# Optimization experiments

Measured on AMD Instinct MI355X. Metric: run time of the kernel, lower is better.

## Reference

```python
import jax, jax.numpy as jnp
from jax import lax
import numpy as np

ALPHA = 100.0  # NetVLAD beta

def _avg_pool2(x):
    # AvgPool2d(2, stride=2) on NCHW
    s = lax.reduce_window(x, 0.0, lax.add, (1, 1, 2, 2), (1, 1, 2, 2), 'VALID')
    return s * 0.25

def _conv3x3(x, w, b):
    y = lax.conv_general_dilated(x, w, (1, 1), 'SAME',
                                 dimension_numbers=('NCHW', 'OIHW', 'NCHW'))
    return y + b[None, :, None, None]

def _l2norm(v, axis):
    return v / jnp.maximum(jnp.linalg.norm(v, axis=axis, keepdims=True), 1e-12)


def setup_inputs() -> dict:
    key = jax.random.key(0)
    ks = jax.random.split(key, 10)
    N, H, W = 16, 512, 512
    K, D = 64, 16          # clusters, NetVLAD feature dim (conv2 out channels)
    T, E, Hd = 64, 300, 512  # caption len, emb dim (rnn_inp=rnn_out), rnn_hid
    img = jax.random.normal(ks[0], (N, 3, H, W), jnp.float32)
    cap = jax.random.normal(ks[1], (N, T, E), jnp.float32)
    conv1_w = jax.random.normal(ks[2], (4, 3, 3, 3), jnp.float32) * 0.1
    conv1_b = jnp.zeros((4,), jnp.float32)
    conv2_w = jax.random.normal(ks[3], (16, 4, 3, 3), jnp.float32) * 0.1
    conv2_b = jnp.zeros((16,), jnp.float32)
    centroids = jax.random.uniform(ks[4], (K, D), jnp.float32)  # torch.rand init
    nv_w = 2.0 * ALPHA * centroids                     # 1x1 conv weight, squeezed [K,D]
    nv_b = -ALPHA * jnp.linalg.norm(centroids, axis=1)  # [K]
    fc_w = jax.random.normal(ks[5], (Hd, K * D), jnp.float32) * 0.02
    fc_b = jnp.zeros((Hd,), jnp.float32)
    hid_w = jax.random.normal(ks[6], (Hd, E + Hd), jnp.float32) * 0.02
    hid_b = jnp.zeros((Hd,), jnp.float32)
    out_w = jax.random.normal(ks[7], (E, Hd), jnp.float32) * 0.02
    out_b = jnp.zeros((E,), jnp.float32)
    return dict(img=img, cap=cap, conv1_w=conv1_w, conv1_b=conv1_b,
                conv2_w=conv2_w, conv2_b=conv2_b, centroids=centroids,
                nv_w=nv_w, nv_b=nv_b, fc_w=fc_w, fc_b=fc_b,
                hid_w=hid_w, hid_b=hid_b, out_w=out_w, out_b=out_b)


def reference(img, cap, conv1_w, conv1_b, conv2_w, conv2_b, centroids,
              nv_w, nv_b, fc_w, fc_b, hid_w, hid_b, out_w, out_b):
    # CNN encoder
    x = jax.nn.relu(_conv3x3(img, conv1_w, conv1_b))
    x = _avg_pool2(x)
    x = jax.nn.relu(_conv3x3(x, conv2_w, conv2_b))
    x = _avg_pool2(x)                      # [N, 16, 128, 128]
    N, C = x.shape[0], x.shape[1]
    xf = x.reshape(N, C, -1)               # [N, C, HW]
    # NetVLAD: 1x1 conv -> softmax over clusters
    soft_assign = jnp.einsum('kc,nch->nkh', nv_w, xf) + nv_b[None, :, None]
    soft_assign = jax.nn.softmax(soft_assign, axis=1)  # [N, K, HW]
    # algebraic two-matmul form of sum_hw a[n,k,hw]*(x[n,c,hw]-centroids[k,c])
    a_sum = soft_assign.sum(axis=-1)                      # [N, K]
    vlad = jnp.einsum('nkh,nch->nkc', soft_assign, xf)    # [N, K, C]
    vlad = vlad - a_sum[:, :, None] * centroids[None]     # [N, K, C]
    vlad = _l2norm(vlad, axis=2)
    vlad = vlad.reshape(N, -1)
    vlad = _l2norm(vlad, axis=1)
    features = vlad @ fc_w.T + fc_b                        # [N, rnn_hid]
    # RNN decoder on sample 0
    feat0 = features[0]
    cap0 = cap[0]                                          # [T, E]

    def step(carry, x_t):
        h, x_in = carry
        comb = jnp.concatenate([x_in, h])
        h_new = jax.nn.sigmoid(hid_w @ comb + hid_b)
        y = jax.nn.sigmoid(out_w @ h_new + out_b)
        return (h_new, x_t), y

    (_, ys) = lax.scan(step, (feat0, cap0[0]), cap0[1:])
    output = jnp.concatenate([cap0[:1], ys], axis=0)       # [T, E]
    loss = jnp.mean((output - cap0) ** 2)
    return loss
```

## Files before the change

kernel.cpp:

```cpp
#include <hip/hip_runtime.h>
#include <math.h>


#define POISON 0xAAAAAAAAu
#define MAGIC  0x13579BDFu

__device__ __forceinline__ float sigmoidf_(float x) {
  return 1.0f / (1.0f + __expf(-x));
}
__device__ __forceinline__ unsigned uld(const unsigned* p) {
  return __hip_atomic_load(p, __ATOMIC_RELAXED, __HIP_MEMORY_SCOPE_AGENT);
}
__device__ __forceinline__ float fld(const float* p) {
  return __hip_atomic_load(p, __ATOMIC_RELAXED, __HIP_MEMORY_SCOPE_AGENT);
}
__device__ __forceinline__ void fst(float* p, float v) {
  __hip_atomic_store(p, v, __ATOMIC_RELAXED, __HIP_MEMORY_SCOPE_AGENT);
}
__device__ __forceinline__ void ust(unsigned* p, unsigned v) {
  __hip_atomic_store(p, v, __ATOMIC_RELAXED, __HIP_MEMORY_SCOPE_AGENT);
}

__global__ __launch_bounds__(256, 1)
void k_front(const float* __restrict__ img,  const float* __restrict__ cap,
             const float* __restrict__ c1w,  const float* __restrict__ c1b,
             const float* __restrict__ c2w,  const float* __restrict__ c2b,
             const float* __restrict__ cent, const float* __restrict__ nvw,
             const float* __restrict__ nvb,  const float* __restrict__ fcw,
             const float* __restrict__ fcb,  const float* __restrict__ hidw,
             const float* __restrict__ hidb,
             float* __restrict__ p1,   float* __restrict__ vacc,
             float* __restrict__ asum, float* __restrict__ feat,
             float* __restrict__ U,    float* __restrict__ H,
             unsigned* __restrict__ flags, float* __restrict__ loss) {
  __shared__ __align__(16) float smem[12832];
  const int bx  = blockIdx.x;
  const int tid = threadIdx.x;
  unsigned* flag_magic = flags + 0;
  unsigned* conv_done  = flags + 1;
  unsigned* vlad_done  = flags + 2;

  if (bx < 63) {
    const int t = bx;
    float* csh = smem;
    if (tid < 256) csh[tid] = cap[t * 300 + tid];
    if (tid < 44) csh[256 + tid] = cap[t * 300 + 256 + tid];
    __syncthreads();
    #pragma unroll
    for (int rr = 0; rr < 2; ++rr) {
      int row = tid + rr * 256;
      float acc = hidb[row];
      const float4* w4 = (const float4*)(hidw + row * 812);
      const float4* c4 = (const float4*)csh;
      #pragma unroll 5
      for (int i = 0; i < 75; ++i) {
        float4 aa = w4[i]; float4 xx = c4[i];
        acc = fmaf(aa.x, xx.x, acc); acc = fmaf(aa.y, xx.y, acc);
        acc = fmaf(aa.z, xx.z, acc); acc = fmaf(aa.w, xx.w, acc);
      }
      U[t * 512 + row] = acc;
    }
    return;
  }

  if (bx < 71) {
    const int q = bx - 63;
    if (tid == 0) {
      while (uld(vlad_done) != 64u) __builtin_amdgcn_s_sleep(8);
    }
    __syncthreads();
    float* v  = smem;
    float* rn = smem + 1024;
    float* fr = smem + 1088;
    for (int i = tid; i < 1024; i += 256)
      v[i] = fld(vacc + i) - fld(asum + (i >> 4)) * cent[i];
    __syncthreads();
    if (tid < 64) {
      float ss = 0.f;
      #pragma unroll
      for (int c = 0; c < 16; ++c) { float xx = v[tid * 16 + c]; ss = fmaf(xx, xx, ss); }
      rn[tid] = fmaxf(sqrtf(ss), 1e-12f);
    }
    __syncthreads();
    float gs = 0.f;
    for (int i = tid; i < 1024; i += 256) {
      float nv = v[i] / rn[i >> 4];
      v[i] = nv;
      gs = fmaf(nv, nv, gs);
    }
    #pragma unroll
    for (int o = 32; o > 0; o >>= 1) gs += __shfl_down(gs, o);
    if ((tid & 63) == 0) fr[tid >> 6] = gs;
    __syncthreads();
    if (tid == 0) {
      float tot = fr[0] + fr[1] + fr[2] + fr[3];
      fr[8] = 1.0f / fmaxf(sqrtf(tot), 1e-12f);
    }
    __syncthreads();
    float invg = fr[8];
    int row = q * 64 + (tid >> 2);
    int cg = tid & 3;
    float acc = 0.f;
    const float4* fw4 = (const float4*)(fcw + row * 1024 + cg * 256);
    const float4* v4  = (const float4*)(v + cg * 256);
    #pragma unroll 4
    for (int i = 0; i < 64; ++i) {
      float4 aa = fw4[i]; float4 xx = v4[i];
      acc = fmaf(aa.x, xx.x, acc); acc = fmaf(aa.y, xx.y, acc);
      acc = fmaf(aa.z, xx.z, acc); acc = fmaf(aa.w, xx.w, acc);
    }
    acc += __shfl_xor(acc, 1);
    acc += __shfl_xor(acc, 2);
    if (cg == 0) feat[row] = fmaf(invg, acc, fcb[row]);
    return;
  }

  if (bx < 135) {
    const int vb = bx - 71;
    float* ps  = smem;
    float* xs  = smem + 8320;
    float* wsh = smem + 10880;
    float* bsh = smem + 11904;
    float* aS  = smem + 11968;
    float* cw  = smem + 12224;
    float* cb  = smem + 12800;
    for (int i = tid; i < 1024; i += 256) wsh[i] = nvw[i];
    if (tid < 64) bsh[tid] = nvb[tid];
    for (int i = tid; i < 576; i += 256) cw[i] = c2w[i];
    if (tid < 16) cb[tid] = c2b[tid];
    if (tid == 0) {
      while (uld(conv_done) != 121u) __builtin_amdgcn_s_sleep(4);
    }
    __syncthreads();
    int ox = tid & 127;
    int oy = vb * 2 + (tid >> 7);
    int y0 = oy * 2 - 1, x0 = ox * 2 - 1;
    float a[16][4];
    #pragma unroll
    for (int oc = 0; oc < 16; ++oc) {
      float bb = cb[oc];
      a[oc][0] = bb; a[oc][1] = bb; a[oc][2] = bb; a[oc][3] = bb;
    }
    #pragma unroll
    for (int ci = 0; ci < 4; ++ci) {
      float P[4][4];
      #pragma unroll
      for (int j = 0; j < 4; ++j) {
        int y = y0 + j;
        #pragma unroll
        for (int i = 0; i < 4; ++i) {
          int x = x0 + i;
          bool ok = ((unsigned)y < 256u) && ((unsigned)x < 256u);
          P[j][i] = ok ? fld(p1 + ci * 65536 + y * 256 + x) : 0.0f;
        }
      }
      #pragma unroll
      for (int oc = 0; oc < 16; ++oc) {
        #pragma unroll
        for (int ky = 0; ky < 3; ++ky) {
          #pragma unroll
          for (int kx = 0; kx < 3; ++kx) {
            float wv = cw[oc * 36 + ci * 9 + ky * 3 + kx];
            a[oc][0] = fmaf(wv, P[ky][kx],         a[oc][0]);
            a[oc][1] = fmaf(wv, P[ky][kx + 1],     a[oc][1]);
            a[oc][2] = fmaf(wv, P[ky + 1][kx],     a[oc][2]);
            a[oc][3] = fmaf(wv, P[ky + 1][kx + 1], a[oc][3]);
          }
        }
      }
    }
    float x[16];
    #pragma unroll
    for (int oc = 0; oc < 16; ++oc)
      x[oc] = 0.25f * (fmaxf(a[oc][0], 0.f) + fmaxf(a[oc][1], 0.f) +
                       fmaxf(a[oc][2], 0.f) + fmaxf(a[oc][3], 0.f));
    float p[64];
    float m = -1e30f;
    #pragma unroll
    for (int k = 0; k < 64; ++k) {
      float acc = bsh[k];
      #pragma unroll
      for (int c = 0; c < 16; ++c) acc = fmaf(wsh[k * 16 + c], x[c], acc);
      p[k] = acc;
      m = fmaxf(m, acc);
    }
    float s = 0.f;
    #pragma unroll
    for (int k = 0; k < 64; ++k) { p[k] = __expf(p[k] - m); s += p[k]; }
    float inv = 1.0f / s;
    #pragma unroll
    for (int k = 0; k < 64; ++k) p[k] *= inv;

    int q = tid >> 6, k = tid & 63;
    float acc[16];
    #pragma unroll
    for (int c = 0; c < 16; ++c) acc[c] = 0.f;
    float accA = 0.f;
    for (int pass = 0; pass < 2; ++pass) {
      __syncthreads();
      if ((tid >> 7) == pass) {
        int tt = tid & 127;
        #pragma unroll
        for (int kk = 0; kk < 64; ++kk) ps[tt * 65 + kk] = p[kk];
        #pragma unroll
        for (int c = 0; c < 16; ++c) xs[tt * 20 + c] = x[c];
      }
      __syncthreads();
      #pragma unroll
      for (int j = 0; j < 32; ++j) {
        int tt = q * 32 + j;
        float pv = ps[tt * 65 + k];
        accA += pv;
        const float4* xv = (const float4*)(xs + tt * 20);
        #pragma unroll
        for (int c4 = 0; c4 < 4; ++c4) {
          float4 xx = xv[c4];
          acc[c4 * 4 + 0] = fmaf(pv, xx.x, acc[c4 * 4 + 0]);
          acc[c4 * 4 + 1] = fmaf(pv, xx.y, acc[c4 * 4 + 1]);
          acc[c4 * 4 + 2] = fmaf(pv, xx.z, acc[c4 * 4 + 2]);
          acc[c4 * 4 + 3] = fmaf(pv, xx.w, acc[c4 * 4 + 3]);
        }
      }
    }
    __syncthreads();
    float* red = ps;
    #pragma unroll
    for (int c = 0; c < 16; ++c) red[tid * 16 + c] = acc[c];
    aS[tid] = accA;
    __syncthreads();
    if (q == 0) {
      float aa = aS[k] + aS[64 + k] + aS[128 + k] + aS[192 + k];
      atomicAdd(&asum[k], aa);
    }
    int k2 = tid >> 2;
    int cgc = (tid & 3) * 4;
    #pragma unroll
    for (int cc = 0; cc < 4; ++cc) {
      int c = cgc + cc;
      float vv = red[(0 * 64 + k2) * 16 + c] + red[(1 * 64 + k2) * 16 + c] +
                 red[(2 * 64 + k2) * 16 + c] + red[(3 * 64 + k2) * 16 + c];
      atomicAdd(&vacc[k2 * 16 + c], vv);
    }
    __syncthreads();
    if (tid == 0)
      __hip_atomic_fetch_add(vlad_done, 1u, __ATOMIC_RELAXED,
                             __HIP_MEMORY_SCOPE_AGENT);
    return;
  }

  {
    const int cbk = bx - 135;
    if (cbk == 120) {
      for (int i = tid; i < 1024; i += 256) fst(vacc + i, 0.f);
      if (tid < 64) fst(asum + tid, 0.f);
      if (tid == 0) { fst(loss, 0.f); ust(conv_done, 0u); ust(vlad_done, 0u); }
      unsigned* Hu = (unsigned*)H;
      for (int i = tid; i < 63 * 512; i += 256) ust(Hu + i, POISON);
      __syncthreads();
      if (tid == 0) ust(flag_magic, MAGIC);
    }
    float* cwsh = smem;
    if (tid < 108) cwsh[tid] = c1w[tid];
    if (tid < 4) cwsh[108 + tid] = c1b[tid];
    __syncthreads();
    for (int o = cbk * 256 + tid; o < 262144; o += 121 * 256) {
      int c  = o >> 16;
      int oy = (o >> 8) & 255;
      int ox = o & 255;
      int y0 = oy * 2 - 1, x0 = ox * 2 - 1;
      float a00, a01, a10, a11;
      a00 = a01 = a10 = a11 = cwsh[108 + c];
      #pragma unroll
      for (int ci = 0; ci < 3; ++ci) {
        float P[4][4];
        #pragma unroll
        for (int j = 0; j < 4; ++j) {
          int y = y0 + j;
          #pragma unroll
          for (int i = 0; i < 4; ++i) {
            int x = x0 + i;
            bool ok = ((unsigned)y < 512u) && ((unsigned)x < 512u);
            P[j][i] = ok ? img[ci * 262144 + y * 512 + x] : 0.0f;
          }
        }
        #pragma unroll
        for (int ky = 0; ky < 3; ++ky) {
          #pragma unroll
          for (int kx = 0; kx < 3; ++kx) {
            float wv = cwsh[c * 27 + ci * 9 + ky * 3 + kx];
            a00 = fmaf(wv, P[ky][kx],         a00);
            a01 = fmaf(wv, P[ky][kx + 1],     a01);
            a10 = fmaf(wv, P[ky + 1][kx],     a10);
            a11 = fmaf(wv, P[ky + 1][kx + 1], a11);
          }
        }
      }
      fst(p1 + o, 0.25f * (fmaxf(a00, 0.f) + fmaxf(a01, 0.f) +
                           fmaxf(a10, 0.f) + fmaxf(a11, 0.f)));
    }
    __syncthreads();
    if (tid == 0) {
      while (uld(flag_magic) != MAGIC) __builtin_amdgcn_s_sleep(2);
      __hip_atomic_fetch_add(conv_done, 1u, __ATOMIC_RELAXED,
                             __HIP_MEMORY_SCOPE_AGENT);
    }
  }
}

__global__ __launch_bounds__(256, 1)
void k_back(const float* __restrict__ hidw, const float* __restrict__ U,
            const float* __restrict__ feat, float* __restrict__ H,
            const float* __restrict__ outw, const float* __restrict__ outb,
            const float* __restrict__ cap,  float* __restrict__ loss) {
  __shared__ __align__(16) float smem[1100];
  const int bx  = blockIdx.x;
  const int tid = threadIdx.x;
  unsigned* Hu = (unsigned*)H;

  if (bx < 8) {
    const int r   = tid >> 2;
    const int cg  = tid & 3;
    const int row = bx * 64 + r;
    float4 wr[32];
    const float4* wp = (const float4*)(hidw + row * 812 + 300 + cg * 128);
    #pragma unroll
    for (int i = 0; i < 32; ++i) wr[i] = wp[i];
    float* buf0 = smem;
    float* buf1 = smem + 544;
    const int w0 = (tid >> 7) * 136 + (tid & 127);
    const int w1 = ((tid + 256) >> 7) * 136 + ((tid + 256) & 127);
    const int wown = (row >> 7) * 136 + (row & 127);
    const bool own0 = ((tid >> 6) == bx);
    const bool own1 = (((tid + 256) >> 6) == bx);
    buf0[w0] = feat[tid];
    buf0[w1] = feat[tid + 256];
    __syncthreads();
    for (int t = 0; t < 63; ++t) {
      const float* bufc = (t & 1) ? buf1 : buf0;
      const float* rb = bufc + cg * 136;
      float uval = (cg == 0) ? U[t * 512 + row] : 0.f;
      float acc = 0.f;
      #pragma unroll
      for (int i = 0; i < 32; ++i) {
        float4 h4 = *(const float4*)(rb + i * 4);
        acc = fmaf(wr[i].x, h4.x, acc);
        acc = fmaf(wr[i].y, h4.y, acc);
        acc = fmaf(wr[i].z, h4.z, acc);
        acc = fmaf(wr[i].w, h4.w, acc);
      }
      acc += __shfl_xor(acc, 1);
      acc += __shfl_xor(acc, 2);
      float hn = 0.f;
      if (cg == 0) {
        hn = sigmoidf_(acc + uval);
        fst(H + t * 512 + row, hn);
      }
      if (t < 62) {
        float* bufn = (t & 1) ? buf0 : buf1;
        if (cg == 0) bufn[wown] = hn;
        const unsigned* src = Hu + t * 512;
        unsigned a0 = 0, a1 = 0;
        do {
          if (!own0) a0 = uld(src + tid);
          if (!own1) a1 = uld(src + tid + 256);
        } while ((!own0 && a0 == POISON) || (!own1 && a1 == POISON));
        if (!own0) bufn[w0] = __uint_as_float(a0);
        if (!own1) bufn[w1] = __uint_as_float(a1);
        __syncthreads();
      }
    }
    return;
  }

  const int t = bx - 8;
  float* hsh = smem;
  float* red = smem + 512;
  if (tid == 0) {
    while (uld(Hu + (size_t)t * 512) == POISON) __builtin_amdgcn_s_sleep(64);
  }
  __syncthreads();
  {
    const unsigned* src = Hu + (size_t)t * 512;
    unsigned a0, a1;
    do {
      a0 = uld(src + tid);
      a1 = uld(src + tid + 256);
    } while (a0 == POISON || a1 == POISON);
    hsh[tid] = __uint_as_float(a0);
    hsh[tid + 256] = __uint_as_float(a1);
  }
  __syncthreads();
  float se = 0.f;
  #pragma unroll
  for (int rr = 0; rr < 2; ++rr) {
    int orow = tid + rr * 256;
    if (orow < 300) {
      float acc = outb[orow];
      const float4* w4 = (const float4*)(outw + orow * 512);
      const float4* h4 = (const float4*)hsh;
      #pragma unroll 4
      for (int i = 0; i < 128; ++i) {
        float4 aa = w4[i]; float4 xx = h4[i];
        acc = fmaf(aa.x, xx.x, acc); acc = fmaf(aa.y, xx.y, acc);
        acc = fmaf(aa.z, xx.z, acc); acc = fmaf(aa.w, xx.w, acc);
      }
      float y = sigmoidf_(acc);
      float d = y - cap[(t + 1) * 300 + orow];
      se = fmaf(d, d, se);
    }
  }
  #pragma unroll
  for (int o = 32; o > 0; o >>= 1) se += __shfl_down(se, o);
  if ((tid & 63) == 0) red[tid >> 6] = se;
  __syncthreads();
  if (tid == 0) {
    float tot = red[0] + red[1] + red[2] + red[3];
    atomicAdd(loss, tot * (1.0f / 19200.0f));
  }
}

extern "C" void kernel_launch(void* const* d_in, const int* in_sizes, int n_in,
                              void* d_out, int out_size, void* d_ws, size_t ws_size,
                              hipStream_t stream) {
  (void)in_sizes; (void)n_in; (void)out_size; (void)ws_size;
  const float* img  = (const float*)d_in[0];
  const float* cap  = (const float*)d_in[1];
  const float* c1w  = (const float*)d_in[2];
  const float* c1b  = (const float*)d_in[3];
  const float* c2w  = (const float*)d_in[4];
  const float* c2b  = (const float*)d_in[5];
  const float* cent = (const float*)d_in[6];
  const float* nvw  = (const float*)d_in[7];
  const float* nvb  = (const float*)d_in[8];
  const float* fcw  = (const float*)d_in[9];
  const float* fcb  = (const float*)d_in[10];
  const float* hidw = (const float*)d_in[11];
  const float* hidb = (const float*)d_in[12];
  const float* outw = (const float*)d_in[13];
  const float* outb = (const float*)d_in[14];

  float* ws   = (float*)d_ws;
  float* p1   = ws;
  float* vacc = ws + 262144;
  float* asum = ws + 263168;
  float* feat = ws + 263232;
  float* U    = ws + 263744;
  float* H    = ws + 296000;
  unsigned* flags = (unsigned*)(ws + 328256);

  k_front<<<256, 256, 0, stream>>>(img, cap, c1w, c1b, c2w, c2b, cent, nvw,
                                   nvb, fcw, fcb, hidw, hidb,
                                   p1, vacc, asum, feat, U, H, flags,
                                   (float*)d_out);
  k_back<<<71, 256, 0, stream>>>(hidw, U, feat, H, outw, outb, cap,
                                 (float*)d_out);
}
```

Baseline: 292.0 us.

## Fuse conv1 into VLAD blocks via shared-memory halo tiles; widen RNN blocks

The separate conv1 blocks, which wrote the pooled conv1 output p1 to global memory and signalled through a conv_done counter, are removed. Each VLAD block now computes its own conv1 halo tile (4 rows plus halo) directly into shared memory before running conv2. This drops the global round trip and the cross-block spin wait, at the cost of recomputing halo rows and using more shared memory. The recurrent decoder also moves to 4 blocks of 512 threads with weights held in registers, and the output blocks use 512 threads with one row per thread, which cuts the number of blocks exchanging the hidden state each step.

```diff
diff --git a/kernel.cpp b/kernel.cpp
--- a/kernel.cpp
+++ b/kernel.cpp
@@ -29,19 +29,29 @@
              const float* __restrict__ nvb,  const float* __restrict__ fcw,
              const float* __restrict__ fcb,  const float* __restrict__ hidw,
              const float* __restrict__ hidb,
-             float* __restrict__ p1,   float* __restrict__ vacc,
-             float* __restrict__ asum, float* __restrict__ feat,
-             float* __restrict__ U,    float* __restrict__ H,
+             float* __restrict__ vacc, float* __restrict__ asum,
+             float* __restrict__ feat, float* __restrict__ U,
+             float* __restrict__ H,
              unsigned* __restrict__ flags, float* __restrict__ loss) {
-  __shared__ __align__(16) float smem[12832];
+  __shared__ __align__(16) float smem[19392];
   const int bx  = blockIdx.x;
   const int tid = threadIdx.x;
   unsigned* flag_magic = flags + 0;
-  unsigned* conv_done  = flags + 1;
-  unsigned* vlad_done  = flags + 2;
-
-  if (bx < 63) {
-    const int t = bx;
+  unsigned* vlad_done  = flags + 1;
+
+  if (bx == 0) {
+    for (int i = tid; i < 1024; i += 256) fst(vacc + i, 0.f);
+    if (tid < 64) fst(asum + tid, 0.f);
+    if (tid == 0) { fst(loss, 0.f); ust(vlad_done, 0u); }
+    unsigned* Hu = (unsigned*)H;
+    for (int i = tid; i < 63 * 512; i += 256) ust(Hu + i, POISON);
+    __syncthreads();
+    if (tid == 0) ust(flag_magic, MAGIC);
+    return;
+  }
+
+  if (bx < 64) {
+    const int t = bx - 1;
     float* csh = smem;
     if (tid < 256) csh[tid] = cap[t * 300 + tid];
     if (tid < 44) csh[256 + tid] = cap[t * 300 + 256 + tid];
@@ -63,8 +73,8 @@
     return;
   }
 
-  if (bx < 71) {
-    const int q = bx - 63;
+  if (bx < 72) {
+    const int q = bx - 64;
     if (tid == 0) {
       while (uld(vlad_done) != 64u) __builtin_amdgcn_s_sleep(8);
     }
@@ -115,44 +125,86 @@
     return;
   }
 
-  if (bx < 135) {
-    const int vb = bx - 71;
-    float* ps  = smem;
-    float* xs  = smem + 8320;
-    float* wsh = smem + 10880;
-    float* bsh = smem + 11904;
-    float* aS  = smem + 11968;
-    float* cw  = smem + 12224;
-    float* cb  = smem + 12800;
+  {
+    const int vb = bx - 72;
+    float* p1sh = smem;
+    float* ps   = smem + 6336;
+    float* xs   = smem + 14656;
+    float* wsh  = smem + 17216;
+    float* bsh  = smem + 18240;
+    float* aS   = smem + 18304;
+    float* cw2  = smem + 18560;
+    float* cb2  = smem + 19136;
+    float* cw1  = smem + 19152;
+    float* cb1  = smem + 19260;
     for (int i = tid; i < 1024; i += 256) wsh[i] = nvw[i];
     if (tid < 64) bsh[tid] = nvb[tid];
-    for (int i = tid; i < 576; i += 256) cw[i] = c2w[i];
-    if (tid < 16) cb[tid] = c2b[tid];
-    if (tid == 0) {
-      while (uld(conv_done) != 121u) __builtin_amdgcn_s_sleep(4);
-    }
-    __syncthreads();
+    for (int i = tid; i < 576; i += 256) cw2[i] = c2w[i];
+    if (tid < 16) cb2[tid] = c2b[tid];
+    if (tid < 108) cw1[tid] = c1w[tid];
+    if (tid >= 108 && tid < 112) cb1[tid - 108] = c1b[tid - 108];
+    __syncthreads();
+
+    for (int f = tid; f < 6192; f += 256) {
+      int c  = f / 1548;
+      int r0 = f - c * 1548;
+      int j  = r0 / 258;
+      int xx = r0 - j * 258;
+      int gy = 4 * vb - 1 + j;
+      int gx = xx - 1;
+      float val = 0.f;
+      if ((unsigned)gy < 256u && (unsigned)gx < 256u) {
+        float bb = cb1[c];
+        float a00 = bb, a01 = bb, a10 = bb, a11 = bb;
+        int y0 = 2 * gy - 1, x0 = 2 * gx - 1;
+        #pragma unroll
+        for (int ci = 0; ci < 3; ++ci) {
+          float P[4][4];
+          #pragma unroll
+          for (int jj = 0; jj < 4; ++jj) {
+            int y = y0 + jj;
+            #pragma unroll
+            for (int ii = 0; ii < 4; ++ii) {
+              int x = x0 + ii;
+              bool ok = ((unsigned)y < 512u) && ((unsigned)x < 512u);
+              P[jj][ii] = ok ? img[ci * 262144 + y * 512 + x] : 0.0f;
+            }
+          }
+          #pragma unroll
+          for (int ky = 0; ky < 3; ++ky) {
+            #pragma unroll
+            for (int kx = 0; kx < 3; ++kx) {
+              float wv = cw1[c * 27 + ci * 9 + ky * 3 + kx];
+              a00 = fmaf(wv, P[ky][kx],         a00);
+              a01 = fmaf(wv, P[ky][kx + 1],     a01);
+              a10 = fmaf(wv, P[ky + 1][kx],     a10);
+              a11 = fmaf(wv, P[ky + 1][kx + 1], a11);
+            }
+          }
+        }
+        val = 0.25f * (fmaxf(a00, 0.f) + fmaxf(a01, 0.f) +
+                       fmaxf(a10, 0.f) + fmaxf(a11, 0.f));
+      }
+      p1sh[c * 1584 + j * 264 + xx] = val;
+    }
+    __syncthreads();
+
     int ox = tid & 127;
-    int oy = vb * 2 + (tid >> 7);
-    int y0 = oy * 2 - 1, x0 = ox * 2 - 1;
+    int oyl = tid >> 7;
     float a[16][4];
     #pragma unroll
     for (int oc = 0; oc < 16; ++oc) {
-      float bb = cb[oc];
+      float bb = cb2[oc];
       a[oc][0] = bb; a[oc][1] = bb; a[oc][2] = bb; a[oc][3] = bb;
     }
     #pragma unroll
     for (int ci = 0; ci < 4; ++ci) {
       float P[4][4];
       #pragma unroll
-      for (int j = 0; j < 4; ++j) {
-        int y = y0 + j;
-        #pragma unroll
-        for (int i = 0; i < 4; ++i) {
-          int x = x0 + i;
-          bool ok = ((unsigned)y < 256u) && ((unsigned)x < 256u);
-          P[j][i] = ok ? fld(p1 + ci * 65536 + y * 256 + x) : 0.0f;
-        }
+      for (int jj = 0; jj < 4; ++jj) {
+        #pragma unroll
+        for (int ii = 0; ii < 4; ++ii)
+          P[jj][ii] = p1sh[ci * 1584 + (2 * oyl + jj) * 264 + 2 * ox + ii];
       }
       #pragma unroll
       for (int oc = 0; oc < 16; ++oc) {
@@ -160,7 +212,7 @@
         for (int ky = 0; ky < 3; ++ky) {
           #pragma unroll
           for (int kx = 0; kx < 3; ++kx) {
-            float wv = cw[oc * 36 + ci * 9 + ky * 3 + kx];
+            float wv = cw2[oc * 36 + ci * 9 + ky * 3 + kx];
             a[oc][0] = fmaf(wv, P[ky][kx],         a[oc][0]);
             a[oc][1] = fmaf(wv, P[ky][kx + 1],     a[oc][1]);
             a[oc][2] = fmaf(wv, P[ky + 1][kx],     a[oc][2]);
@@ -174,6 +226,7 @@
     for (int oc = 0; oc < 16; ++oc)
       x[oc] = 0.25f * (fmaxf(a[oc][0], 0.f) + fmaxf(a[oc][1], 0.f) +
                        fmaxf(a[oc][2], 0.f) + fmaxf(a[oc][3], 0.f));
+
     float p[64];
     float m = -1e30f;
     #pragma unroll
@@ -228,6 +281,10 @@
     for (int c = 0; c < 16; ++c) red[tid * 16 + c] = acc[c];
     aS[tid] = accA;
     __syncthreads();
+    if (tid == 0) {
+      while (uld(flag_magic) != MAGIC) __builtin_amdgcn_s_sleep(2);
+    }
+    __syncthreads();
     if (q == 0) {
       float aa = aS[k] + aS[64 + k] + aS[128 + k] + aS[192 + k];
       atomicAdd(&asum[k], aa);
@@ -245,69 +302,10 @@
     if (tid == 0)
       __hip_atomic_fetch_add(vlad_done, 1u, __ATOMIC_RELAXED,
                              __HIP_MEMORY_SCOPE_AGENT);
-    return;
-  }
-
-  {
-    const int cbk = bx - 135;
-    if (cbk == 120) {
-      for (int i = tid; i < 1024; i += 256) fst(vacc + i, 0.f);
-      if (tid < 64) fst(asum + tid, 0.f);
-      if (tid == 0) { fst(loss, 0.f); ust(conv_done, 0u); ust(vlad_done, 0u); }
-      unsigned* Hu = (unsigned*)H;
-      for (int i = tid; i < 63 * 512; i += 256) ust(Hu + i, POISON);
-      __syncthreads();
-      if (tid == 0) ust(flag_magic, MAGIC);
-    }
-    float* cwsh = smem;
-    if (tid < 108) cwsh[tid] = c1w[tid];
-    if (tid < 4) cwsh[108 + tid] = c1b[tid];
-    __syncthreads();
-    for (int o = cbk * 256 + tid; o < 262144; o += 121 * 256) {
-      int c  = o >> 16;
-      int oy = (o >> 8) & 255;
-      int ox = o & 255;
-      int y0 = oy * 2 - 1, x0 = ox * 2 - 1;
-      float a00, a01, a10, a11;
-      a00 = a01 = a10 = a11 = cwsh[108 + c];
-      #pragma unroll
-      for (int ci = 0; ci < 3; ++ci) {
-        float P[4][4];
-        #pragma unroll
-        for (int j = 0; j < 4; ++j) {
-          int y = y0 + j;
-          #pragma unroll
-          for (int i = 0; i < 4; ++i) {
-            int x = x0 + i;
-            bool ok = ((unsigned)y < 512u) && ((unsigned)x < 512u);
-            P[j][i] = ok ? img[ci * 262144 + y * 512 + x] : 0.0f;
-          }
-        }
-        #pragma unroll
-        for (int ky = 0; ky < 3; ++ky) {
-          #pragma unroll
-          for (int kx = 0; kx < 3; ++kx) {
-            float wv = cwsh[c * 27 + ci * 9 + ky * 3 + kx];
-            a00 = fmaf(wv, P[ky][kx],         a00);
-            a01 = fmaf(wv, P[ky][kx + 1],     a01);
-            a10 = fmaf(wv, P[ky + 1][kx],     a10);
-            a11 = fmaf(wv, P[ky + 1][kx + 1], a11);
-          }
-        }
-      }
-      fst(p1 + o, 0.25f * (fmaxf(a00, 0.f) + fmaxf(a01, 0.f) +
-                           fmaxf(a10, 0.f) + fmaxf(a11, 0.f)));
-    }
-    __syncthreads();
-    if (tid == 0) {
-      while (uld(flag_magic) != MAGIC) __builtin_amdgcn_s_sleep(2);
-      __hip_atomic_fetch_add(conv_done, 1u, __ATOMIC_RELAXED,
-                             __HIP_MEMORY_SCOPE_AGENT);
-    }
-  }
-}
-
-__global__ __launch_bounds__(256, 1)
+  }
+}
+
+__global__ __launch_bounds__(512, 1)
 void k_back(const float* __restrict__ hidw, const float* __restrict__ U,
             const float* __restrict__ feat, float* __restrict__ H,
             const float* __restrict__ outw, const float* __restrict__ outb,
@@ -317,36 +315,40 @@
   const int tid = threadIdx.x;
   unsigned* Hu = (unsigned*)H;
 
-  if (bx < 8) {
+  if (bx < 4) {
     const int r   = tid >> 2;
     const int cg  = tid & 3;
-    const int row = bx * 64 + r;
-    float4 wr[32];
-    const float4* wp = (const float4*)(hidw + row * 812 + 300 + cg * 128);
-    #pragma unroll
-    for (int i = 0; i < 32; ++i) wr[i] = wp[i];
+    const int row = bx * 128 + r;
+    float wrf[128];
+    {
+      const float4* wp = (const float4*)(hidw + row * 812 + 300 + cg * 128);
+      #pragma unroll
+      for (int i = 0; i < 32; ++i) {
+        float4 tm = wp[i];
+        wrf[4 * i + 0] = tm.x; wrf[4 * i + 1] = tm.y;
+        wrf[4 * i + 2] = tm.z; wrf[4 * i + 3] = tm.w;
+      }
+    }
+    #pragma unroll
+    for (int i = 0; i < 128; ++i) asm volatile("" : "+v"(wrf[i]));
     float* buf0 = smem;
     float* buf1 = smem + 544;
-    const int w0 = (tid >> 7) * 136 + (tid & 127);
-    const int w1 = ((tid + 256) >> 7) * 136 + ((tid + 256) & 127);
-    const int wown = (row >> 7) * 136 + (row & 127);
-    const bool own0 = ((tid >> 6) == bx);
-    const bool own1 = (((tid + 256) >> 6) == bx);
-    buf0[w0] = feat[tid];
-    buf0[w1] = feat[tid + 256];
+    const int wz = (tid >> 7) * 136 + (tid & 127);
+    const int wown = ((row >> 7) * 136) + (row & 127);
+    const bool own = ((tid >> 7) == bx);
+    buf0[wz] = feat[tid];
     __syncthreads();
     for (int t = 0; t < 63; ++t) {
-      const float* bufc = (t & 1) ? buf1 : buf0;
-      const float* rb = bufc + cg * 136;
+      const float* rb = ((t & 1) ? buf1 : buf0) + cg * 136;
       float uval = (cg == 0) ? U[t * 512 + row] : 0.f;
       float acc = 0.f;
       #pragma unroll
       for (int i = 0; i < 32; ++i) {
         float4 h4 = *(const float4*)(rb + i * 4);
-        acc = fmaf(wr[i].x, h4.x, acc);
-        acc = fmaf(wr[i].y, h4.y, acc);
-        acc = fmaf(wr[i].z, h4.z, acc);
-        acc = fmaf(wr[i].w, h4.w, acc);
+        acc = fmaf(wrf[4 * i + 0], h4.x, acc);
+        acc = fmaf(wrf[4 * i + 1], h4.y, acc);
+        acc = fmaf(wrf[4 * i + 2], h4.z, acc);
+        acc = fmaf(wrf[4 * i + 3], h4.w, acc);
       }
       acc += __shfl_xor(acc, 1);
       acc += __shfl_xor(acc, 2);
@@ -358,63 +360,59 @@
       if (t < 62) {
         float* bufn = (t & 1) ? buf0 : buf1;
         if (cg == 0) bufn[wown] = hn;
-        const unsigned* src = Hu + t * 512;
-        unsigned a0 = 0, a1 = 0;
-        do {
-          if (!own0) a0 = uld(src + tid);
-          if (!own1) a1 = uld(src + tid + 256);
-        } while ((!own0 && a0 == POISON) || (!own1 && a1 == POISON));
-        if (!own0) bufn[w0] = __uint_as_float(a0);
-        if (!own1) bufn[w1] = __uint_as_float(a1);
+        if (!own) {
+          const unsigned* src = Hu + t * 512 + tid;
+          unsigned aa;
+          do {
+            aa = uld(src);
+          } while (aa == POISON);
+          bufn[wz] = __uint_as_float(aa);
+        }
         __syncthreads();
       }
     }
     return;
   }
 
-  const int t = bx - 8;
+  const int t = bx - 4;
   float* hsh = smem;
   float* red = smem + 512;
   if (tid == 0) {
-    while (uld(Hu + (size_t)t * 512) == POISON) __builtin_amdgcn_s_sleep(64);
+    while (uld(Hu + (size_t)t * 512) == POISON) __builtin_amdgcn_s_sleep(32);
   }
   __syncthreads();
   {
-    const unsigned* src = Hu + (size_t)t * 512;
-    unsigned a0, a1;
+    const unsigned* src = Hu + (size_t)t * 512 + tid;
+    unsigned aa;
     do {
-      a0 = uld(src + tid);
-      a1 = uld(src + tid + 256);
-    } while (a0 == POISON || a1 == POISON);
-    hsh[tid] = __uint_as_float(a0);
-    hsh[tid + 256] = __uint_as_float(a1);
+      aa = uld(src);
+    } while (aa == POISON);
+    hsh[tid] = __uint_as_float(aa);
   }
   __syncthreads();
   float se = 0.f;
-  #pragma unroll
-  for (int rr = 0; rr < 2; ++rr) {
-    int orow = tid + rr * 256;
-    if (orow < 300) {
-      float acc = outb[orow];
-      const float4* w4 = (const float4*)(outw + orow * 512);
-      const float4* h4 = (const float4*)hsh;
-      #pragma unroll 4
-      for (int i = 0; i < 128; ++i) {
-        float4 aa = w4[i]; float4 xx = h4[i];
-        acc = fmaf(aa.x, xx.x, acc); acc = fmaf(aa.y, xx.y, acc);
-        acc = fmaf(aa.z, xx.z, acc); acc = fmaf(aa.w, xx.w, acc);
-      }
-      float y = sigmoidf_(acc);
-      float d = y - cap[(t + 1) * 300 + orow];
-      se = fmaf(d, d, se);
-    }
+  if (tid < 300) {
+    float acc = outb[tid];
+    const float4* w4 = (const float4*)(outw + tid * 512);
+    const float4* h4 = (const float4*)hsh;
+    #pragma unroll 4
+    for (int i = 0; i < 128; ++i) {
+      float4 aa = w4[i]; float4 xx = h4[i];
+      acc = fmaf(aa.x, xx.x, acc); acc = fmaf(aa.y, xx.y, acc);
+      acc = fmaf(aa.z, xx.z, acc); acc = fmaf(aa.w, xx.w, acc);
+    }
+    float y = sigmoidf_(acc);
+    float d = y - cap[(t + 1) * 300 + tid];
+    se = fmaf(d, d, se);
   }
   #pragma unroll
   for (int o = 32; o > 0; o >>= 1) se += __shfl_down(se, o);
   if ((tid & 63) == 0) red[tid >> 6] = se;
   __syncthreads();
   if (tid == 0) {
-    float tot = red[0] + red[1] + red[2] + red[3];
+    float tot = 0.f;
+    #pragma unroll
+    for (int qq = 0; qq < 8; ++qq) tot += red[qq];
     atomicAdd(loss, tot * (1.0f / 19200.0f));
   }
 }
@@ -440,18 +438,17 @@
   const float* outb = (const float*)d_in[14];
 
   float* ws   = (float*)d_ws;
-  float* p1   = ws;
-  float* vacc = ws + 262144;
-  float* asum = ws + 263168;
-  float* feat = ws + 263232;
-  float* U    = ws + 263744;
-  float* H    = ws + 296000;
-  unsigned* flags = (unsigned*)(ws + 328256);
-
-  k_front<<<256, 256, 0, stream>>>(img, cap, c1w, c1b, c2w, c2b, cent, nvw,
+  float* vacc = ws;
+  float* asum = ws + 1024;
+  float* feat = ws + 1088;
+  float* U    = ws + 1600;
+  float* H    = ws + 33856;
+  unsigned* flags = (unsigned*)(ws + 66112);
+
+  k_front<<<136, 256, 0, stream>>>(img, cap, c1w, c1b, c2w, c2b, cent, nvw,
                                    nvb, fcw, fcb, hidw, hidb,
-                                   p1, vacc, asum, feat, U, H, flags,
+                                   vacc, asum, feat, U, H, flags,
                                    (float*)d_out);
-  k_back<<<71, 256, 0, stream>>>(hidw, U, feat, H, outw, outb, cap,
+  k_back<<<67, 512, 0, stream>>>(hidw, U, feat, H, outw, outb, cap,
                                  (float*)d_out);
 }
```

Result: no change. 287.8 us (-1.4%).
